# Optimization experiments

Hardware: AMD Instinct MI355X
Metric: run time of the kernel (lower is better)

The kernel has to match this reference:

```python
import jax, jax.numpy as jnp
import numpy as np
import math

D_MODEL = 512
N_HEADS = 8
D_K = D_MODEL // N_HEADS
B, S, KC = 16, 1024, 32
NEG = -1e32


def setup_inputs() -> dict:
    key = jax.random.key(0)
    ks = jax.random.split(key, 14)
    s = 1.0 / math.sqrt(D_MODEL)
    return {
        "q": jax.random.normal(ks[0], (B, S, D_MODEL), jnp.float32),
        "k": jax.random.normal(ks[1], (B, S, D_MODEL), jnp.float32),
        "v": jax.random.normal(ks[2], (B, S, D_MODEL), jnp.float32),
        "q_seq": jax.random.randint(ks[3], (B, S), 0, 500, jnp.int32),
        "c_seq": jax.random.randint(ks[4], (B, S, KC), 0, 2, jnp.int32),
        "Wq": jax.random.normal(ks[5], (D_MODEL, D_MODEL), jnp.float32) * s,
        "bq": jnp.zeros((D_MODEL,), jnp.float32),
        "Wk": jax.random.normal(ks[6], (D_MODEL, D_MODEL), jnp.float32) * s,
        "bk": jnp.zeros((D_MODEL,), jnp.float32),
        "Wv": jax.random.normal(ks[7], (D_MODEL, D_MODEL), jnp.float32) * s,
        "bv": jnp.zeros((D_MODEL,), jnp.float32),
        "Wo": jax.random.normal(ks[8], (D_MODEL, D_MODEL), jnp.float32) * s,
        "bo": jnp.zeros((D_MODEL,), jnp.float32),
    }


def qc_mask(q_seq, c_seq):
    # maskq[b,i,j] = 1 if same question id
    maskq = (q_seq[:, :, None] == q_seq[:, None, :]).astype(jnp.int32)
    # maskc[b,i,j] = 1 if any shared concept; entries are {0,1} so AND-sum == dot
    overlap = jnp.einsum("bik,bjk->bij", c_seq, c_seq)  # int32
    maskc = (overlap > 0).astype(jnp.int32)
    # strict lower triangle: 1 - triu(ones, k=0)
    tri = jnp.tril(jnp.ones((S, S), jnp.int32), k=-1)[None]
    return (maskc + maskq + 1) * tri  # values in {0,1,2,3}


def reference(q, k, v, q_seq, c_seq, Wq, bq, Wk, bk, Wv, bv, Wo, bo):
    bs = q.shape[0]
    # NOTE: original code swaps the linears: k<-k_linear(k), q<-v_linear(q), v<-q_linear(v)
    kh = (k @ Wk.T + bk).reshape(bs, S, N_HEADS, D_K).transpose(0, 2, 1, 3)
    qh = (q @ Wv.T + bv).reshape(bs, S, N_HEADS, D_K).transpose(0, 2, 1, 3)
    vh = (v @ Wq.T + bq).reshape(bs, S, N_HEADS, D_K).transpose(0, 2, 1, 3)

    mask = qc_mask(q_seq, c_seq)  # [B,S,S] int
    scores = jnp.einsum("bhid,bhjd->bhij", qh, kh) / math.sqrt(D_K)
    m = mask[:, None]  # [B,1,S,S]
    scores = jnp.where(m == 0, NEG, scores)
    scores = jax.nn.softmax(scores, axis=-1)

    adjustments = jnp.array([0.0, 0.5, 1.0, 2.0], jnp.float32)
    adjusted = scores * adjustments[m]
    sums = jnp.sum(scores, axis=-1, keepdims=True)
    sums = jnp.where(sums == 0, jnp.ones_like(sums), sums)
    adjusted = adjusted / sums

    out = jnp.einsum("bhij,bhjd->bhid", adjusted, vh)
    concat = out.transpose(0, 2, 1, 3).reshape(bs, S, D_MODEL)
    return concat @ Wo.T + bo
```

## Files before the change

### kernel.cpp

```cpp
#include <hip/hip_runtime.h>
#include <stdint.h>

typedef unsigned short u16;
typedef unsigned int   u32;
typedef unsigned long long u64;
typedef __attribute__((ext_vector_type(8)))  short short8;
typedef __attribute__((ext_vector_type(4)))  float f32x4;
typedef __attribute__((ext_vector_type(16))) float f32x16;
typedef __attribute__((ext_vector_type(4)))  unsigned int u32x4;

__device__ __forceinline__ u16 f2bf(float f) {
  u32 u = __builtin_bit_cast(u32, f);
  u32 r = u + 0x7FFFu + ((u >> 16) & 1u);
  return (u16)(r >> 16);
}

__device__ __forceinline__ u32 cvtpk(float a, float b) {
  u32 r;
  asm("v_cvt_pk_bf16_f32 %0, %1, %2" : "=v"(r) : "v"(a), "v"(b));
  return r;
}

__device__ __forceinline__ void gload_lds16(const void* g, void* l) {
  __builtin_amdgcn_global_load_lds(
      (__attribute__((address_space(1))) void*)(uintptr_t)g,
      (__attribute__((address_space(3))) void*)(u32)(uintptr_t)l,
      16, 0, 0);
}

#define SB() __builtin_amdgcn_sched_barrier(0)

__global__ void cast4_kernel(const float* __restrict__ s0, const float* __restrict__ s1,
                             const float* __restrict__ s2, const float* __restrict__ s3,
                             u16* __restrict__ d0, u16* __restrict__ d1,
                             u16* __restrict__ d2, u16* __restrict__ d3, int n8) {
  const int sel = blockIdx.y;
  const float* src = sel == 0 ? s0 : sel == 1 ? s1 : sel == 2 ? s2 : s3;
  u16* dst = sel == 0 ? d0 : sel == 1 ? d1 : sel == 2 ? d2 : d3;
  int i = blockIdx.x * blockDim.x + threadIdx.x;
  if (i >= n8) return;
  const float4* s4 = (const float4*)src;
  float4 x = s4[2 * (size_t)i];
  float4 y = s4[2 * (size_t)i + 1];
  u32x4 r;
  r.x = cvtpk(x.x, x.y); r.y = cvtpk(x.z, x.w);
  r.z = cvtpk(y.x, y.y); r.w = cvtpk(y.z, y.w);
  *(u32x4*)(dst + 8 * (size_t)i) = r;
}

__global__ void pack_kernel(const int* __restrict__ q_seq, const int* __restrict__ c_seq,
                            int2* __restrict__ meta, int n) {
  int i = blockIdx.x * blockDim.x + threadIdx.x;
  if (i >= n) return;
  u32 bits = 0;
#pragma unroll
  for (int j = 0; j < 32; ++j)
    bits |= (c_seq[(size_t)i * 32 + j] != 0) ? (1u << j) : 0u;
  meta[i] = make_int2(q_seq[i], (int)bits);
}

__global__ __launch_bounds__(256) void mask_kernel(const int2* __restrict__ meta,
                                                   u64* __restrict__ maskw) {
  const int qc = blockIdx.x, kt = blockIdx.y, b = blockIdx.z;
  const int t = threadIdx.x;
  const int q = qc * 256 + t;
  __shared__ int2 colm[32];
  if (t < 32) colm[t] = meta[b * 1024 + kt * 32 + t];
  __syncthreads();
  const int2 qm = meta[b * 1024 + q];
  const int rs = qm.x; const u32 rb = (u32)qm.y;
  u64 w = 0;
#pragma unroll
  for (int j = 0; j < 32; ++j) {
    const int2 cm = colm[j];
    const int kj = kt * 32 + j;
    u32 m = 0;
    if (kj < q) m = 1u + (rs == cm.x ? 1u : 0u) + (((rb & (u32)cm.y) != 0u) ? 1u : 0u);
    w |= (u64)m << (2 * j);
  }
  maskw[((size_t)b * 32 + kt) * 1024 + q] = w;
}

__global__ __launch_bounds__(256) void gemm_qkv(const float* __restrict__ qf,
                                                const float* __restrict__ kf,
                                                const float* __restrict__ vf,
                                                const u16* __restrict__ Wvb,
                                                const u16* __restrict__ Wkb,
                                                const u16* __restrict__ Wqb,
                                                const float* __restrict__ bv,
                                                const float* __restrict__ bk,
                                                const float* __restrict__ bq,
                                                u16* __restrict__ qhb,
                                                u16* __restrict__ khb,
                                                u16* __restrict__ vTb,
                                                float kscale) {
  const int sel = blockIdx.y;
  const float* Af   = sel == 0 ? qf : sel == 1 ? kf : vf;
  const u16*   W    = sel == 0 ? Wvb : sel == 1 ? Wkb : Wqb;
  const float* bias = sel == 0 ? bv : sel == 1 ? bk : bq;
  const float scale = sel == 1 ? kscale : 1.0f;
  const int K = 512;

  __shared__ __align__(16) u16 As[128 * 64];
  __shared__ __align__(16) u16 Bs[128 * 64];
  const int t    = threadIdx.x;
  const int lane = t & 63;
  const int wid  = t >> 6;
  const int g    = lane >> 4, l15 = lane & 15;
  const int wm   = wid >> 1, wn = wid & 1;
  const int wrk  = (blockIdx.x & 7) * 64 + (blockIdx.x >> 3);
  const int mb   = wrk >> 2, nbi = wrk & 3;
  const int m0   = mb << 7, n0 = nbi << 7;
  const int srow = t >> 3;
  const int scol = (((t & 7) ^ (srow & 7)) << 3);
  const int dcol = ((t & 7) << 3);
  const int rsw  = l15 & 7;

  f32x4 acc[4][4];
#pragma unroll
  for (int i = 0; i < 4; ++i)
#pragma unroll
    for (int j = 0; j < 4; ++j) acc[i][j] = f32x4{0.f, 0.f, 0.f, 0.f};

  float4 ax[4], ay[4];
#pragma unroll
  for (int i = 0; i < 4; ++i) {
    const float* src = Af + (size_t)(m0 + 32 * i + srow) * K + scol;
    ax[i] = *(const float4*)src;
    ay[i] = *(const float4*)(src + 4);
  }

  for (int k0 = 0; k0 < K; k0 += 64) {
    SB();
    __builtin_amdgcn_s_barrier();
    SB();
#pragma unroll
    for (int i = 0; i < 4; ++i)
      gload_lds16(W + (size_t)(n0 + i * 32 + srow) * K + k0 + scol,
                  Bs + i * 2048 + t * 8);
#pragma unroll
    for (int i = 0; i < 4; ++i) {
      u32x4 r;
      r.x = cvtpk(ax[i].x, ax[i].y); r.y = cvtpk(ax[i].z, ax[i].w);
      r.z = cvtpk(ay[i].x, ay[i].y); r.w = cvtpk(ay[i].z, ay[i].w);
      *(u32x4*)(As + (32 * i + srow) * 64 + dcol) = r;
    }
    SB();
    const int kn = (k0 + 64) & (K - 1);
#pragma unroll
    for (int i = 0; i < 4; ++i) {
      const float* src = Af + (size_t)(m0 + 32 * i + srow) * K + kn + scol;
      ax[i] = *(const float4*)src;
      ay[i] = *(const float4*)(src + 4);
    }
    SB();
    asm volatile("s_waitcnt vmcnt(8) lgkmcnt(0)" ::: "memory");
    __builtin_amdgcn_s_barrier();
    SB();
#pragma unroll
    for (int kk = 0; kk < 2; ++kk) {
      short8 a[4], b[4];
#pragma unroll
      for (int mi = 0; mi < 4; ++mi)
        a[mi] = *(const short8*)(As + (wm * 64 + mi * 16 + l15) * 64
                                 + (((kk * 4 + g) ^ rsw) << 3));
#pragma unroll
      for (int ni = 0; ni < 4; ++ni)
        b[ni] = *(const short8*)(Bs + (wn * 64 + ni * 16 + l15) * 64
                                 + (((kk * 4 + g) ^ rsw) << 3));
#pragma unroll
      for (int mi = 0; mi < 4; ++mi)
#pragma unroll
        for (int ni = 0; ni < 4; ++ni)
          acc[mi][ni] = __builtin_amdgcn_mfma_f32_16x16x32_bf16(a[mi], b[ni], acc[mi][ni], 0, 0, 0);
    }
  }
  asm volatile("s_waitcnt vmcnt(0)" ::: "memory");

#pragma unroll
  for (int ni = 0; ni < 4; ++ni) {
    const int col = n0 + wn * 64 + ni * 16 + l15;
    const float bz = bias[col];
#pragma unroll
    for (int mi = 0; mi < 4; ++mi) {
#pragma unroll
      for (int r = 0; r < 4; ++r) {
        const int row = m0 + wm * 64 + mi * 16 + g * 4 + r;
        const u16 val = f2bf((acc[mi][ni][r] + bz) * scale);
        const size_t base = ((size_t)(row >> 10) * 8 + (col >> 6)) * 65536;
        const int s = row & 1023, d = col & 63;
        if (sel == 0) {
          qhb[base + (size_t)s * 64 + d] = val;
        } else if (sel == 1) {
          khb[base + (s >> 5) * 2048 + (d >> 3) * 256 + (s & 31) * 8 + (d & 7)] = val;
        } else {
          vTb[base + (s >> 3) * 512 + d * 8 + (s & 7)] = val;
        }
      }
    }
  }
}

__global__ __launch_bounds__(256) void gemm_out(const u16* __restrict__ A,
                                                const u16* __restrict__ W,
                                                const float* __restrict__ bias,
                                                float* __restrict__ outp) {
  const int K = 512, N = 512;
  __shared__ __align__(16) u16 As[128 * 64];
  __shared__ __align__(16) u16 Bs[128 * 64];
  const int t    = threadIdx.x;
  const int lane = t & 63;
  const int wid  = t >> 6;
  const int g    = lane >> 4, l15 = lane & 15;
  const int wm   = wid >> 1, wn = wid & 1;
  const int wrk  = (blockIdx.x & 7) * 64 + (blockIdx.x >> 3);
  const int mb   = wrk >> 2, nbi = wrk & 3;
  const int m0   = mb << 7, n0 = nbi << 7;
  const int srow = t >> 3;
  const int scol = (((t & 7) ^ (srow & 7)) << 3);
  const int rsw  = l15 & 7;

  f32x4 acc[4][4];
#pragma unroll
  for (int i = 0; i < 4; ++i)
#pragma unroll
    for (int j = 0; j < 4; ++j) acc[i][j] = f32x4{0.f, 0.f, 0.f, 0.f};

  for (int k0 = 0; k0 < K; k0 += 64) {
    SB();
    __builtin_amdgcn_s_barrier();
    SB();
#pragma unroll
    for (int i = 0; i < 4; ++i) {
      gload_lds16(A + (size_t)(m0 + i * 32 + srow) * K + k0 + scol, As + i * 2048 + t * 8);
      gload_lds16(W + (size_t)(n0 + i * 32 + srow) * K + k0 + scol, Bs + i * 2048 + t * 8);
    }
    SB();
    asm volatile("s_waitcnt vmcnt(0)" ::: "memory");
    __builtin_amdgcn_s_barrier();
    SB();
#pragma unroll
    for (int kk = 0; kk < 2; ++kk) {
      short8 a[4], b[4];
#pragma unroll
      for (int mi = 0; mi < 4; ++mi)
        a[mi] = *(const short8*)(As + (wm * 64 + mi * 16 + l15) * 64
                                 + (((kk * 4 + g) ^ rsw) << 3));
#pragma unroll
      for (int ni = 0; ni < 4; ++ni)
        b[ni] = *(const short8*)(Bs + (wn * 64 + ni * 16 + l15) * 64
                                 + (((kk * 4 + g) ^ rsw) << 3));
#pragma unroll
      for (int mi = 0; mi < 4; ++mi)
#pragma unroll
        for (int ni = 0; ni < 4; ++ni)
          acc[mi][ni] = __builtin_amdgcn_mfma_f32_16x16x32_bf16(a[mi], b[ni], acc[mi][ni], 0, 0, 0);
    }
  }

#pragma unroll
  for (int ni = 0; ni < 4; ++ni) {
    const int col = n0 + wn * 64 + ni * 16 + l15;
    const float bz = bias[col];
#pragma unroll
    for (int mi = 0; mi < 4; ++mi)
#pragma unroll
      for (int r = 0; r < 4; ++r) {
        const int row = m0 + wm * 64 + mi * 16 + g * 4 + r;
        outp[(size_t)row * N + col] = acc[mi][ni][r] + bz;
      }
  }
}

__global__ __launch_bounds__(256, 2) void attn_kernel(const u16* __restrict__ qh,
                                                      const u16* __restrict__ kh,
                                                      const u16* __restrict__ vT,
                                                      const u64* __restrict__ maskw,
                                                      u16* __restrict__ outc) {
  const int h  = blockIdx.x;
  const int qp = blockIdx.y;
  const int b  = blockIdx.z;
  const int lane = threadIdx.x & 63;
  const int wid  = threadIdx.x >> 6;
  const int pair = wid >> 1, p = wid & 1;
  const int l31 = lane & 31;
  const int hh  = lane >> 5;
  const int hh8 = hh << 3, fourh = hh << 2, eighth = hh << 3;
  const int jt = pair ? (31 - qp) : qp;
  const int q0 = jt << 5;
  const int qi = q0 + l31;
  const size_t bh = (size_t)b * 8 + h;
  const u16* Q  = qh + bh * 65536;
  const u16* Kp = kh + bh * 65536;
  const u16* Vt = vT + bh * 65536;
  const u64* mrow = maskw + (size_t)b * 32768 + qi;

  __shared__ float mO[2][32][64];
  __shared__ float mL[2][64];
  __shared__ __align__(16) float Sl[2][32];

  short8 qB[4];
#pragma unroll
  for (int i = 0; i < 4; ++i)
    qB[i] = *(const short8*)(Q + (size_t)qi * 64 + i * 16 + eighth);

  f32x16 O0, O1;
#pragma unroll
  for (int i = 0; i < 16; ++i) { O0[i] = 0.f; O1[i] = 0.f; }
  float lr[4] = {0.f, 0.f, 0.f, 0.f};

  const int nt = jt + 1;

#define LOADK(dst, tt)                                                        \
  { _Pragma("unroll")                                                         \
    for (int i = 0; i < 4; ++i)                                               \
      dst[i] = *(const short8*)(Kp + (tt) * 2048 + ((2 * i + hh) * 32 + l31) * 8); }

#define SOFTMAX(S, wm, pkk)                                                   \
  { const u32 wsh0 = ((u32)(wm)) >> hh8;                                      \
    const u32 wsh1 = ((u32)((wm) >> 32)) >> hh8;                              \
    _Pragma("unroll")                                                         \
    for (int s = 0; s < 4; ++s) {                                             \
      const u32 wsel = (s < 2) ? wsh0 : wsh1;                                 \
      float pv[4];                                                            \
      _Pragma("unroll")                                                       \
      for (int r = 0; r < 4; ++r) {                                           \
        const int m = 4 * s + r;                                              \
        const u32 m2 = (wsel >> (2 * r + 16 * (s & 1))) & 3u;                 \
        float e;                                                              \
        asm("v_exp_f32 %0, %1" : "=v"(e) : "v"((S)[m]));                      \
        const float pp = (m2 != 0u) ? e : 0.f;                                \
        lr[r] += pp;                                                          \
        asm("v_ldexp_f32 %0, %1, %2" : "=v"(pv[r]) : "v"(pp), "v"(m2));       \
      }                                                                       \
      pkk[2 * s]     = cvtpk(pv[0], pv[1]);                                   \
      pkk[2 * s + 1] = cvtpk(pv[2], pv[3]);                                   \
    } }

#define PVSTEP(pkk, tt)                                                       \
  { _Pragma("unroll")                                                         \
    for (int t4 = 0; t4 < 2; ++t4) {                                          \
      u32 a0 = pkk[4 * t4 + 0], b0 = pkk[4 * t4 + 2];                         \
      u32 a1 = pkk[4 * t4 + 1], b1 = pkk[4 * t4 + 3];                         \
      asm("v_permlane32_swap_b32 %0, %1" : "+v"(a0), "+v"(b0));               \
      asm("v_permlane32_swap_b32 %0, %1" : "+v"(a1), "+v"(b1));               \
      u32x4 w; w.x = a0; w.y = a1; w.z = b0; w.w = b1;                        \
      const short8 pa = __builtin_bit_cast(short8, w);                        \
      const short8 v0 = *(const short8*)(Vt + (size_t)((tt) * 4 + t4 * 2 + hh) * 512 + l31 * 8); \
      const short8 v1 = *(const short8*)(Vt + (size_t)((tt) * 4 + t4 * 2 + hh) * 512 + (32 + l31) * 8); \
      O0 = __builtin_amdgcn_mfma_f32_32x32x16_bf16(pa, v0, O0, 0, 0, 0);      \
      O1 = __builtin_amdgcn_mfma_f32_32x32x16_bf16(pa, v1, O1, 0, 0, 0);      \
    } }

  short8 kAa[4], kAb[4];
  LOADK(kAa, p);
  LOADK(kAb, (p + 2));
  u64 wma = mrow[(size_t)p << 10];
  u64 wmb = mrow[(size_t)(p + 2) << 10];

  int t = p;
  while (t < nt) {
    const bool two = (t + 2) < nt;

    f32x16 Sa;
#pragma unroll
    for (int i = 0; i < 16; ++i) Sa[i] = 0.f;
#pragma unroll
    for (int i = 0; i < 4; ++i)
      Sa = __builtin_amdgcn_mfma_f32_32x32x16_bf16(kAa[i], qB[i], Sa, 0, 0, 0);
    f32x16 Sb;
#pragma unroll
    for (int i = 0; i < 16; ++i) Sb[i] = 0.f;
    if (two) {
#pragma unroll
      for (int i = 0; i < 4; ++i)
        Sb = __builtin_amdgcn_mfma_f32_32x32x16_bf16(kAb[i], qB[i], Sb, 0, 0, 0);
    }

    const int tn = t + (two ? 4 : 2);
    u64 wman = 0, wmbn = 0;
    if (tn < nt) {
      LOADK(kAa, tn);
      wman = mrow[(size_t)tn << 10];
      if (tn + 2 < nt) {
        LOADK(kAb, (tn + 2));
        wmbn = mrow[(size_t)(tn + 2) << 10];
      }
    }

    u32 pka[8], pkb[8];
    SOFTMAX(Sa, wma, pka);
    if (two) SOFTMAX(Sb, wmb, pkb);

    PVSTEP(pka, t);
    if (two) PVSTEP(pkb, (t + 2));

    wma = wman; wmb = wmbn;
    t = tn;
  }

#undef LOADK
#undef SOFTMAX
#undef PVSTEP

  float lrun = (lr[0] + lr[1]) + (lr[2] + lr[3]);

  if (p == 1) {
#pragma unroll
    for (int r = 0; r < 16; ++r) {
      mO[pair][r][lane]      = O0[r];
      mO[pair][16 + r][lane] = O1[r];
    }
    mL[pair][lane] = lrun;
  }
  __syncthreads();
  if (p == 0) {
#pragma unroll
    for (int r = 0; r < 16; ++r) {
      O0[r] += mO[pair][r][lane];
      O1[r] += mO[pair][16 + r][lane];
    }
    lrun += mL[pair][lane];

    const float ssum = lrun + __shfl_xor(lrun, 32);
    if (lane < 32) Sl[pair][l31] = (ssum > 0.f) ? 0.25f / ssum : 0.f;
    __builtin_amdgcn_sched_barrier(0);
    asm volatile("s_waitcnt lgkmcnt(0)" ::: "memory");
    __builtin_amdgcn_sched_barrier(0);
#pragma unroll
    for (int t2 = 0; t2 < 4; ++t2) {
      const float4 inv4 = *(const float4*)&Sl[pair][8 * t2 + fourh];
#pragma unroll
      for (int r = 0; r < 4; ++r) {
        const int m = 4 * t2 + r;
        const float iv = (r == 0) ? inv4.x : (r == 1) ? inv4.y : (r == 2) ? inv4.z : inv4.w;
        const int qrow = q0 + 8 * t2 + fourh + r;
        u16* op = outc + ((size_t)b * 1024 + qrow) * 512 + h * 64;
        op[l31]      = f2bf(O0[m] * iv);
        op[32 + l31] = f2bf(O1[m] * iv);
      }
    }
  }
}

extern "C" void kernel_launch(void* const* d_in, const int* in_sizes, int n_in,
                              void* d_out, int out_size, void* d_ws, size_t ws_size,
                              hipStream_t stream) {
  (void)in_sizes; (void)n_in; (void)out_size; (void)ws_size;
  const float* q    = (const float*)d_in[0];
  const float* k    = (const float*)d_in[1];
  const float* v    = (const float*)d_in[2];
  const int*  q_seq = (const int*)d_in[3];
  const int*  c_seq = (const int*)d_in[4];
  const float* Wq   = (const float*)d_in[5];
  const float* bq   = (const float*)d_in[6];
  const float* Wk   = (const float*)d_in[7];
  const float* bk   = (const float*)d_in[8];
  const float* Wv   = (const float*)d_in[9];
  const float* bv   = (const float*)d_in[10];
  const float* Wo   = (const float*)d_in[11];
  const float* bo   = (const float*)d_in[12];
  float* out = (float*)d_out;

  char* ws = (char*)d_ws;
  const size_t SZH = 16ull * 8 * 1024 * 64 * 2;
  u16* qhb   = (u16*)(ws + 0 * SZH);
  u16* khb   = (u16*)(ws + 1 * SZH);
  u16* vTb   = (u16*)(ws + 2 * SZH);
  u16* attnc = (u16*)(ws + 3 * SZH);
  u16* Wvb = (u16*)(ws + 4 * SZH + 0 * 524288);
  u16* Wkb = (u16*)(ws + 4 * SZH + 1 * 524288);
  u16* Wqb = (u16*)(ws + 4 * SZH + 2 * 524288);
  u16* Wob = (u16*)(ws + 4 * SZH + 3 * 524288);
  int2* meta  = (int2*)(ws + 4 * SZH + 4 * 524288);
  u64* maskw  = (u64*)(ws + 4 * SZH + 4 * 524288 + 131072);

  const int n8w = 512 * 512 / 8;
  cast4_kernel<<<dim3(n8w / 256, 4), 256, 0, stream>>>(Wv, Wk, Wq, Wo,
                                                       Wvb, Wkb, Wqb, Wob, n8w);
  pack_kernel<<<64, 256, 0, stream>>>(q_seq, c_seq, meta, 16384);
  mask_kernel<<<dim3(4, 32, 16), 256, 0, stream>>>(meta, maskw);

  const float KSCALE = 0.18033688011112042f;
  gemm_qkv<<<dim3(512, 3), 256, 0, stream>>>(q, k, v, Wvb, Wkb, Wqb,
                                             bv, bk, bq, qhb, khb, vTb, KSCALE);
  attn_kernel<<<dim3(8, 16, 16), 256, 0, stream>>>(qhb, khb, vTb, maskw, attnc);
  gemm_out<<<512, 256, 0, stream>>>(attnc, Wob, bo, out);
}
```

Baseline: 140.1 us.

## Restructure projection GEMMs to keep full-K A row block resident in LDS

```diff
diff --git a/kernel.cpp b/kernel.cpp
--- a/kernel.cpp
+++ b/kernel.cpp
@@ -81,195 +81,195 @@
   maskw[((size_t)b * 32 + kt) * 1024 + q] = w;
 }
 
-__global__ __launch_bounds__(256) void gemm_qkv(const float* __restrict__ qf,
-                                                const float* __restrict__ kf,
-                                                const float* __restrict__ vf,
-                                                const u16* __restrict__ Wvb,
-                                                const u16* __restrict__ Wkb,
-                                                const u16* __restrict__ Wqb,
-                                                const float* __restrict__ bv,
-                                                const float* __restrict__ bk,
-                                                const float* __restrict__ bq,
-                                                u16* __restrict__ qhb,
-                                                u16* __restrict__ khb,
-                                                u16* __restrict__ vTb,
-                                                float kscale) {
-  const int sel = blockIdx.y;
-  const float* Af   = sel == 0 ? qf : sel == 1 ? kf : vf;
-  const u16*   W    = sel == 0 ? Wvb : sel == 1 ? Wkb : Wqb;
-  const float* bias = sel == 0 ? bv : sel == 1 ? bk : bq;
-  const float scale = sel == 1 ? kscale : 1.0f;
-  const int K = 512;
-
-  __shared__ __align__(16) u16 As[128 * 64];
-  __shared__ __align__(16) u16 Bs[128 * 64];
+__global__ __launch_bounds__(256, 2) void gemm_qkv(const float* __restrict__ qf,
+                                                   const float* __restrict__ kf,
+                                                   const float* __restrict__ vf,
+                                                   const u16* __restrict__ Wvb,
+                                                   const u16* __restrict__ Wkb,
+                                                   const u16* __restrict__ Wqb,
+                                                   const float* __restrict__ bv,
+                                                   const float* __restrict__ bk,
+                                                   const float* __restrict__ bq,
+                                                   u16* __restrict__ qhb,
+                                                   u16* __restrict__ khb,
+                                                   u16* __restrict__ vTb,
+                                                   float kscale) {
+  __shared__ __align__(16) u16 Alds[64 * 512];
+  __shared__ __align__(16) u16 Bb[2][64 * 64];
   const int t    = threadIdx.x;
   const int lane = t & 63;
   const int wid  = t >> 6;
   const int g    = lane >> 4, l15 = lane & 15;
-  const int wm   = wid >> 1, wn = wid & 1;
-  const int wrk  = (blockIdx.x & 7) * 64 + (blockIdx.x >> 3);
-  const int mb   = wrk >> 2, nbi = wrk & 3;
-  const int m0   = mb << 7, n0 = nbi << 7;
-  const int srow = t >> 3;
-  const int scol = (((t & 7) ^ (srow & 7)) << 3);
-  const int dcol = ((t & 7) << 3);
-  const int rsw  = l15 & 7;
-
-  f32x4 acc[4][4];
-#pragma unroll
-  for (int i = 0; i < 4; ++i)
-#pragma unroll
-    for (int j = 0; j < 4; ++j) acc[i][j] = f32x4{0.f, 0.f, 0.f, 0.f};
-
-  float4 ax[4], ay[4];
-#pragma unroll
-  for (int i = 0; i < 4; ++i) {
-    const float* src = Af + (size_t)(m0 + 32 * i + srow) * K + scol;
-    ax[i] = *(const float4*)src;
-    ay[i] = *(const float4*)(src + 4);
-  }
-
-  for (int k0 = 0; k0 < K; k0 += 64) {
-    SB();
+  const int mb   = blockIdx.x;
+  const int which = mb >> 8;
+  const float* Ax   = which == 0 ? qf : which == 1 ? kf : vf;
+  const u16*   W    = which == 0 ? Wvb : which == 1 ? Wkb : Wqb;
+  const float* bias = which == 0 ? bv : which == 1 ? bk : bq;
+  const float scale = which == 1 ? kscale : 1.0f;
+  u16* outb = which == 0 ? qhb : which == 1 ? khb : vTb;
+  const int mloc = (mb & 255) << 6;
+
+  const int arow = wid * 16 + l15;
+  const int ar7  = arow & 7;
+
+#pragma unroll
+  for (int j = 0; j < 16; ++j) {
+    const int u = j * 256 + t;
+    const int row = u >> 6;
+    const int slot = u & 63;
+    const float* src = Ax + (size_t)(mloc + row) * 512 + slot * 8;
+    const float4 x = *(const float4*)src;
+    const float4 y = *(const float4*)(src + 4);
+    u32x4 r;
+    r.x = cvtpk(x.x, x.y); r.y = cvtpk(x.z, x.w);
+    r.z = cvtpk(y.x, y.y); r.w = cvtpk(y.z, y.w);
+    *(u32x4*)(&Alds[row * 512 + ((slot ^ (row & 7)) << 3)]) = r;
+  }
+
+#define STAGE_B(nb, kt, buf)                                                  \
+  { _Pragma("unroll")                                                         \
+    for (int i2 = 0; i2 < 2; ++i2) {                                          \
+      const int u2 = i2 * 256 + t;                                            \
+      const int bc = u2 >> 3, bs = u2 & 7;                                    \
+      gload_lds16(W + (size_t)((nb) * 64 + bc) * 512 + (kt) * 64             \
+                    + ((bs ^ (bc & 7)) << 3),                                 \
+                  &Bb[buf][u2 * 8]);                                          \
+    } }
+
+  STAGE_B(0, 0, 0);
+  __syncthreads();
+
+  f32x4 acc[4];
+#pragma unroll
+  for (int j = 0; j < 4; ++j) acc[j] = f32x4{0.f, 0.f, 0.f, 0.f};
+
+  for (int s = 0; s < 64; ++s) {
+    const int cur = s & 1;
+    const int sn = (s + 1) & 63;
+    STAGE_B(sn >> 3, sn & 7, cur ^ 1);
+    SB();
+    const int kt = s & 7;
+#pragma unroll
+    for (int kk = 0; kk < 2; ++kk) {
+      const int sA = kt * 8 + kk * 4 + g;
+      const short8 a = *(const short8*)(&Alds[arow * 512 + ((sA ^ ar7) << 3)]);
+#pragma unroll
+      for (int ni = 0; ni < 4; ++ni) {
+        const int bcol = ni * 16 + l15;
+        const int sBp = ((kk * 4 + g) ^ (bcol & 7)) << 3;
+        const short8 b = *(const short8*)(&Bb[cur][bcol * 64 + sBp]);
+        acc[ni] = __builtin_amdgcn_mfma_f32_16x16x32_bf16(a, b, acc[ni], 0, 0, 0);
+      }
+    }
+    if (kt == 7) {
+      const int nbi = s >> 3;
+#pragma unroll
+      for (int ni = 0; ni < 4; ++ni) {
+        const int col = nbi * 64 + ni * 16 + l15;
+        const float bz = bias[col];
+#pragma unroll
+        for (int r = 0; r < 4; ++r) {
+          const int row = mloc + wid * 16 + g * 4 + r;
+          const u16 val = f2bf((acc[ni][r] + bz) * scale);
+          const size_t base = ((size_t)(row >> 10) * 8 + (col >> 6)) * 65536;
+          const int ss = row & 1023, d = col & 63;
+          if (which == 0) {
+            outb[base + (size_t)ss * 64 + d] = val;
+          } else if (which == 1) {
+            outb[base + (ss >> 5) * 2048 + (d >> 3) * 256 + (ss & 31) * 8 + (d & 7)] = val;
+          } else {
+            outb[base + (ss >> 3) * 512 + d * 8 + (ss & 7)] = val;
+          }
+          acc[ni][r] = 0.f;
+        }
+      }
+    }
+    SB();
+    asm volatile("s_waitcnt vmcnt(0)" ::: "memory");
     __builtin_amdgcn_s_barrier();
     SB();
-#pragma unroll
-    for (int i = 0; i < 4; ++i)
-      gload_lds16(W + (size_t)(n0 + i * 32 + srow) * K + k0 + scol,
-                  Bs + i * 2048 + t * 8);
-#pragma unroll
-    for (int i = 0; i < 4; ++i) {
-      u32x4 r;
-      r.x = cvtpk(ax[i].x, ax[i].y); r.y = cvtpk(ax[i].z, ax[i].w);
-      r.z = cvtpk(ay[i].x, ay[i].y); r.w = cvtpk(ay[i].z, ay[i].w);
-      *(u32x4*)(As + (32 * i + srow) * 64 + dcol) = r;
-    }
-    SB();
-    const int kn = (k0 + 64) & (K - 1);
-#pragma unroll
-    for (int i = 0; i < 4; ++i) {
-      const float* src = Af + (size_t)(m0 + 32 * i + srow) * K + kn + scol;
-      ax[i] = *(const float4*)src;
-      ay[i] = *(const float4*)(src + 4);
-    }
-    SB();
-    asm volatile("s_waitcnt vmcnt(8) lgkmcnt(0)" ::: "memory");
-    __builtin_amdgcn_s_barrier();
-    SB();
-#pragma unroll
-    for (int kk = 0; kk < 2; ++kk) {
-      short8 a[4], b[4];
-#pragma unroll
-      for (int mi = 0; mi < 4; ++mi)
-        a[mi] = *(const short8*)(As + (wm * 64 + mi * 16 + l15) * 64
-                                 + (((kk * 4 + g) ^ rsw) << 3));
-#pragma unroll
-      for (int ni = 0; ni < 4; ++ni)
-        b[ni] = *(const short8*)(Bs + (wn * 64 + ni * 16 + l15) * 64
-                                 + (((kk * 4 + g) ^ rsw) << 3));
-#pragma unroll
-      for (int mi = 0; mi < 4; ++mi)
-#pragma unroll
-        for (int ni = 0; ni < 4; ++ni)
-          acc[mi][ni] = __builtin_amdgcn_mfma_f32_16x16x32_bf16(a[mi], b[ni], acc[mi][ni], 0, 0, 0);
-    }
-  }
-  asm volatile("s_waitcnt vmcnt(0)" ::: "memory");
-
-#pragma unroll
-  for (int ni = 0; ni < 4; ++ni) {
-    const int col = n0 + wn * 64 + ni * 16 + l15;
-    const float bz = bias[col];
-#pragma unroll
-    for (int mi = 0; mi < 4; ++mi) {
-#pragma unroll
-      for (int r = 0; r < 4; ++r) {
-        const int row = m0 + wm * 64 + mi * 16 + g * 4 + r;
-        const u16 val = f2bf((acc[mi][ni][r] + bz) * scale);
-        const size_t base = ((size_t)(row >> 10) * 8 + (col >> 6)) * 65536;
-        const int s = row & 1023, d = col & 63;
-        if (sel == 0) {
-          qhb[base + (size_t)s * 64 + d] = val;
-        } else if (sel == 1) {
-          khb[base + (s >> 5) * 2048 + (d >> 3) * 256 + (s & 31) * 8 + (d & 7)] = val;
-        } else {
-          vTb[base + (s >> 3) * 512 + d * 8 + (s & 7)] = val;
-        }
-      }
-    }
-  }
-}
-
-__global__ __launch_bounds__(256) void gemm_out(const u16* __restrict__ A,
-                                                const u16* __restrict__ W,
-                                                const float* __restrict__ bias,
-                                                float* __restrict__ outp) {
-  const int K = 512, N = 512;
-  __shared__ __align__(16) u16 As[128 * 64];
-  __shared__ __align__(16) u16 Bs[128 * 64];
+  }
+#undef STAGE_B
+}
+
+__global__ __launch_bounds__(256, 2) void gemm_out(const u16* __restrict__ A,
+                                                   const u16* __restrict__ W,
+                                                   const float* __restrict__ bias,
+                                                   float* __restrict__ outp) {
+  __shared__ __align__(16) u16 Alds[64 * 512];
+  __shared__ __align__(16) u16 Bb[2][64 * 64];
   const int t    = threadIdx.x;
   const int lane = t & 63;
   const int wid  = t >> 6;
   const int g    = lane >> 4, l15 = lane & 15;
-  const int wm   = wid >> 1, wn = wid & 1;
-  const int wrk  = (blockIdx.x & 7) * 64 + (blockIdx.x >> 3);
-  const int mb   = wrk >> 2, nbi = wrk & 3;
-  const int m0   = mb << 7, n0 = nbi << 7;
-  const int srow = t >> 3;
-  const int scol = (((t & 7) ^ (srow & 7)) << 3);
-  const int rsw  = l15 & 7;
-
-  f32x4 acc[4][4];
-#pragma unroll
-  for (int i = 0; i < 4; ++i)
-#pragma unroll
-    for (int j = 0; j < 4; ++j) acc[i][j] = f32x4{0.f, 0.f, 0.f, 0.f};
-
-  for (int k0 = 0; k0 < K; k0 += 64) {
-    SB();
-    __builtin_amdgcn_s_barrier();
-    SB();
-#pragma unroll
-    for (int i = 0; i < 4; ++i) {
-      gload_lds16(A + (size_t)(m0 + i * 32 + srow) * K + k0 + scol, As + i * 2048 + t * 8);
-      gload_lds16(W + (size_t)(n0 + i * 32 + srow) * K + k0 + scol, Bs + i * 2048 + t * 8);
+  const int mloc = blockIdx.x << 6;
+  const int arow = wid * 16 + l15;
+  const int ar7  = arow & 7;
+
+#pragma unroll
+  for (int j = 0; j < 16; ++j) {
+    const int u = j * 256 + t;
+    const int row = u >> 6;
+    const int slot = u & 63;
+    gload_lds16(A + (size_t)(mloc + row) * 512 + ((slot ^ (row & 7)) << 3),
+                &Alds[u * 8]);
+  }
+
+#define STAGE_B(nb, kt, buf)                                                  \
+  { _Pragma("unroll")                                                         \
+    for (int i2 = 0; i2 < 2; ++i2) {                                          \
+      const int u2 = i2 * 256 + t;                                            \
+      const int bc = u2 >> 3, bs = u2 & 7;                                    \
+      gload_lds16(W + (size_t)((nb) * 64 + bc) * 512 + (kt) * 64             \
+                    + ((bs ^ (bc & 7)) << 3),                                 \
+                  &Bb[buf][u2 * 8]);                                          \
+    } }
+
+  STAGE_B(0, 0, 0);
+  __syncthreads();
+
+  f32x4 acc[4];
+#pragma unroll
+  for (int j = 0; j < 4; ++j) acc[j] = f32x4{0.f, 0.f, 0.f, 0.f};
+
+  for (int s = 0; s < 64; ++s) {
+    const int cur = s & 1;
+    const int sn = (s + 1) & 63;
+    STAGE_B(sn >> 3, sn & 7, cur ^ 1);
+    SB();
+    const int kt = s & 7;
+#pragma unroll
+    for (int kk = 0; kk < 2; ++kk) {
+      const int sA = kt * 8 + kk * 4 + g;
+      const short8 a = *(const short8*)(&Alds[arow * 512 + ((sA ^ ar7) << 3)]);
+#pragma unroll
+      for (int ni = 0; ni < 4; ++ni) {
+        const int bcol = ni * 16 + l15;
+        const int sBp = ((kk * 4 + g) ^ (bcol & 7)) << 3;
+        const short8 b = *(const short8*)(&Bb[cur][bcol * 64 + sBp]);
+        acc[ni] = __builtin_amdgcn_mfma_f32_16x16x32_bf16(a, b, acc[ni], 0, 0, 0);
+      }
+    }
+    if (kt == 7) {
+      const int nbi = s >> 3;
+#pragma unroll
+      for (int ni = 0; ni < 4; ++ni) {
+        const int col = nbi * 64 + ni * 16 + l15;
+        const float bz = bias[col];
+#pragma unroll
+        for (int r = 0; r < 4; ++r) {
+          const int row = mloc + wid * 16 + g * 4 + r;
+          outp[(size_t)row * 512 + col] = acc[ni][r] + bz;
+          acc[ni][r] = 0.f;
+        }
+      }
     }
     SB();
     asm volatile("s_waitcnt vmcnt(0)" ::: "memory");
     __builtin_amdgcn_s_barrier();
     SB();
-#pragma unroll
-    for (int kk = 0; kk < 2; ++kk) {
-      short8 a[4], b[4];
-#pragma unroll
-      for (int mi = 0; mi < 4; ++mi)
-        a[mi] = *(const short8*)(As + (wm * 64 + mi * 16 + l15) * 64
-                                 + (((kk * 4 + g) ^ rsw) << 3));
-#pragma unroll
-      for (int ni = 0; ni < 4; ++ni)
-        b[ni] = *(const short8*)(Bs + (wn * 64 + ni * 16 + l15) * 64
-                                 + (((kk * 4 + g) ^ rsw) << 3));
-#pragma unroll
-      for (int mi = 0; mi < 4; ++mi)
-#pragma unroll
-        for (int ni = 0; ni < 4; ++ni)
-          acc[mi][ni] = __builtin_amdgcn_mfma_f32_16x16x32_bf16(a[mi], b[ni], acc[mi][ni], 0, 0, 0);
-    }
-  }
-
-#pragma unroll
-  for (int ni = 0; ni < 4; ++ni) {
-    const int col = n0 + wn * 64 + ni * 16 + l15;
-    const float bz = bias[col];
-#pragma unroll
-    for (int mi = 0; mi < 4; ++mi)
-#pragma unroll
-      for (int r = 0; r < 4; ++r) {
-        const int row = m0 + wm * 64 + mi * 16 + g * 4 + r;
-        outp[(size_t)row * N + col] = acc[mi][ni][r] + bz;
-      }
-  }
+  }
+#undef STAGE_B
 }
 
 __global__ __launch_bounds__(256, 2) void attn_kernel(const u16* __restrict__ qh,
@@ -482,8 +482,8 @@
   mask_kernel<<<dim3(4, 32, 16), 256, 0, stream>>>(meta, maskw);
 
   const float KSCALE = 0.18033688011112042f;
-  gemm_qkv<<<dim3(512, 3), 256, 0, stream>>>(q, k, v, Wvb, Wkb, Wqb,
-                                             bv, bk, bq, qhb, khb, vTb, KSCALE);
+  gemm_qkv<<<dim3(768), 256, 0, stream>>>(q, k, v, Wvb, Wkb, Wqb,
+                                          bv, bk, bq, qhb, khb, vTb, KSCALE);
   attn_kernel<<<dim3(8, 16, 16), 256, 0, stream>>>(qhb, khb, vTb, maskw, attnc);
-  gemm_out<<<512, 256, 0, stream>>>(attnc, Wob, bo, out);
-}
+  gemm_out<<<dim3(256), 256, 0, stream>>>(attnc, Wob, bo, out);
+}
```

New measurement: 199.1 us. 42.2% more time.
